# Performance work log

Measured on AMD Instinct MI355X. Metric: run time of the kernel, lower is better.

Reference implementation:

```python
import jax, jax.numpy as jnp
import numpy as np

GRID_SIZE = 64            # scene grid cells at pitch
PITCH = 0.02              # data['resolution']
RES = 0.04                # mast3r_grid_resolution
MAX_PTS = 16              # max_points_in_voxel
MIN_PTS = 15              # min_points_in_voxel
G = int(round(GRID_SIZE * PITCH / RES))   # mast3r grid cells per dim = 32
NUM_VOX = G * G * G                       # 32768
N = 8 * 384 * 512                         # num_images * H * W flattened points


def setup_inputs():
    key = jax.random.key(0)
    k1, k2, k3, k4, k5 = jax.random.split(key, 5)
    half = GRID_SIZE * PITCH / 2 * 1.25   # sample slightly beyond cube -> some out-of-bounds
    pts_0 = jax.random.uniform(k1, (N, 3), jnp.float32, -half, half)
    pts_conf = jax.random.uniform(k2, (N, 1), jnp.float32)
    pts_desc = jax.random.normal(k3, (N, 24), jnp.float32)
    pts_desc_conf = jax.random.uniform(k4, (N, 1), jnp.float32)
    image_ids = jax.random.randint(k5, (N,), 0, 16, jnp.int32)
    center = jnp.zeros((3,), jnp.float32)
    occupancy_grid = jnp.zeros((1, G, G, G), jnp.int32)
    return {"pts_0": pts_0, "pts_conf": pts_conf, "pts_desc": pts_desc,
            "pts_desc_conf": pts_desc_conf, "image_ids": image_ids,
            "center": center, "occupancy_grid": occupancy_grid}


def _voxelize(pts_0, pts_conf, pts_desc, pts_desc_conf, image_ids, center):
    # Hard voxelization with per-voxel point cap, confidence-priority ordering.
    # Fixed-shape (jit-friendly) version: dropped points are masked (zeroed / -1),
    # sentinel bucket NUM_VOX holds out-of-bounds / filtered points.
    n = pts_0.shape[0]
    cube = GRID_SIZE * PITCH
    min_corner = center - cube / 2
    idx = jnp.floor((pts_0 - min_corner) / RES).astype(jnp.int32)
    in_b = jnp.all((idx >= 0) & (idx < G), axis=-1)
    vid = idx[:, 0] * (G * G) + idx[:, 1] * G + idx[:, 2]
    vid = jnp.where(in_b, vid, NUM_VOX)
    ones = jnp.ones((n,), jnp.int32)
    counts0 = jax.ops.segment_sum(ones, vid, num_segments=NUM_VOX + 1)  # bincount
    keep = in_b & (counts0[vid] > MIN_PTS)      # min_points_in_voxel filter
    vid = jnp.where(keep, vid, NUM_VOX)
    # local coords normalized to [-1, 1] within the voxel
    pts_local = (pts_0 - min_corner - idx.astype(pts_0.dtype) * RES - RES / 2) / (RES / 2)
    # stable sort by confidence, descending
    order1 = jnp.argsort(-pts_conf[:, 0], stable=True)
    conf_sorted = pts_conf[order1]
    vid1 = vid[order1]
    # stable sort by voxel id, ascending -> within a voxel, points ordered by conf
    order2 = jnp.argsort(vid1, stable=True)
    vid_sorted = vid1[order2]
    point_sorted = order1[order2]               # indices into original point arrays
    counts = jax.ops.segment_sum(ones, vid_sorted, num_segments=NUM_VOX + 1)
    offsets = jnp.cumsum(counts) - counts
    pos = jnp.arange(n, dtype=jnp.int32) - offsets[vid_sorted].astype(jnp.int32)
    valid = (pos < MAX_PTS) & (vid_sorted < NUM_VOX)   # cap points per voxel
    row = jnp.where(valid, vid_sorted, NUM_VOX)
    col = jnp.clip(pos, 0, MAX_PTS - 1)
    table = jnp.full((NUM_VOX + 1, MAX_PTS), -1, jnp.int32)
    table = table.at[row, col].set(jnp.arange(n, dtype=jnp.int32))[:NUM_VOX]
    vf = valid.astype(pts_0.dtype)
    pts_out = pts_local[point_sorted] * vf[:, None]
    # faithful to source quirk: conf was sorted in place then indexed by point ids
    conf_out = conf_sorted[point_sorted] * vf[:, None]
    desc_out = pts_desc[point_sorted] * vf[:, None]
    desc_conf_out = pts_desc_conf[point_sorted] * vf[:, None]
    img_out = jnp.where(valid, image_ids[point_sorted], -1)
    occupied = (table[:, 0] >= 0).astype(jnp.int32)    # padded analogue of voxel_ids_final
    return pts_out, conf_out, desc_out, desc_conf_out, table, occupied, img_out


def reference(pts_0, pts_conf, pts_desc, pts_desc_conf, image_ids, center, occupancy_grid):
    X = _voxelize(pts_0, pts_conf, pts_desc, pts_desc_conf, image_ids, center)
    return X + (occupancy_grid,)
```

## Files before the change

kernel.cpp:

```cpp
#include <hip/hip_runtime.h>


#define NG 32
#define NVOXEL 32768
#define TILE 4096
#define VCAP 8192
#define CCAP 8192

typedef float v4f __attribute__((ext_vector_type(4)));

__device__ __forceinline__ int conf_bucket(float c) {
  int b = (int)(c * 65536.0f);
  return b < 0 ? 0 : (b > 65535 ? 65535 : b);
}

__device__ int block_scan_excl(int v, int* lds) {
  int t = threadIdx.x;
  lds[t] = v;
  __syncthreads();
  for (int off = 1; off < (int)blockDim.x; off <<= 1) {
    int x = (t >= off) ? lds[t - off] : 0;
    __syncthreads();
    lds[t] += x;
    __syncthreads();
  }
  int incl = lds[t];
  __syncthreads();
  return incl - v;
}

__global__ __launch_bounds__(256) void k_hist(int n, const float* __restrict__ pts,
                                              const float* __restrict__ conf,
                                              const float* __restrict__ center,
                                              unsigned short* __restrict__ code,
                                              int* __restrict__ blockHistV,
                                              int* __restrict__ blockHistC) {
  __shared__ int vh[256], ch[256];
  int t = threadIdx.x;
  vh[t] = 0; ch[t] = 0;
  __syncthreads();
  int base = blockIdx.x * TILE;
  float mx = center[0] - 0.64f, my = center[1] - 0.64f, mz = center[2] - 0.64f;
  for (int r = 0; r < TILE; r += 256) {
    int p = base + r + t;
    if (p < n) {
      float x = pts[3 * p], y = pts[3 * p + 1], z = pts[3 * p + 2];
      int ix = (int)floorf((x - mx) / 0.04f);
      int iy = (int)floorf((y - my) / 0.04f);
      int iz = (int)floorf((z - mz) / 0.04f);
      bool inb = (ix >= 0 && ix < NG && iy >= 0 && iy < NG && iz >= 0 && iz < NG);
      int vid = inb ? (ix * 1024 + iy * 32 + iz) : 0xFFFF;
      code[p] = (unsigned short)vid;
      if (inb) atomicAdd(&vh[vid >> 7], 1);
      atomicAdd(&ch[conf_bucket(conf[p]) >> 8], 1);
    }
  }
  __syncthreads();
  blockHistV[blockIdx.x * 256 + t] = vh[t];
  blockHistC[blockIdx.x * 256 + t] = ch[t];
}

__global__ void k_binprefix(int nblk, const int* __restrict__ blockHistV,
                            const int* __restrict__ blockHistC, int* __restrict__ blockBaseV,
                            int* __restrict__ blockBaseC, int* __restrict__ totals) {
  __shared__ int lds[512];
  int t = threadIdx.x;
  int bin = blockIdx.x & 255;
  int isConf = blockIdx.x >> 8;
  const int* src = isConf ? blockHistC : blockHistV;
  int* dst = isConf ? blockBaseC : blockBaseV;
  int v = (t < nblk) ? src[t * 256 + bin] : 0;
  int ex = block_scan_excl(v, lds);
  if (t < nblk) dst[t * 256 + bin] = ex;
  if (t == nblk - 1) totals[blockIdx.x] = ex + v;
}

__global__ __launch_bounds__(256) void k_scatter(int n, const unsigned short* __restrict__ code,
                                                 const float* __restrict__ conf,
                                                 const int* __restrict__ totals,
                                                 const int* __restrict__ blockBaseV,
                                                 const int* __restrict__ blockBaseC,
                                                 uint2* __restrict__ vidSeg,
                                                 float* __restrict__ confSeg) {
  __shared__ int curV[256], curC[256], lds[256];
  int t = threadIdx.x;
  int exV = block_scan_excl(totals[t], lds);
  int exC = block_scan_excl(totals[256 + t], lds);
  curV[t] = exV + blockBaseV[blockIdx.x * 256 + t];
  curC[t] = exC + blockBaseC[blockIdx.x * 256 + t];
  __syncthreads();
  int base = blockIdx.x * TILE;
  for (int r = 0; r < TILE; r += 256) {
    int p = base + r + t;
    if (p < n) {
      int vid = code[p];
      float c = conf[p];
      int cb = conf_bucket(c);
      if (vid != 0xFFFF) {
        int loc = atomicAdd(&curV[vid >> 7], 1);
        vidSeg[loc] = make_uint2(((unsigned)p << 7) | (unsigned)(vid & 127),
                                 __float_as_uint(c));
      }
      int loc2 = atomicAdd(&curC[cb >> 8], 1);
      confSeg[loc2] = c;
    }
  }
}

__global__ __launch_bounds__(256) void k_voxconf(int n, const uint2* __restrict__ vidSeg,
                                                 const float* __restrict__ confSeg,
                                                 const int* __restrict__ totals,
                                                 uint2* __restrict__ ptlist2,
                                                 int* __restrict__ counts0,
                                                 int* __restrict__ rawOff,
                                                 float* __restrict__ confSorted) {
  __shared__ uint2 seg[VCAP];
  __shared__ int cnt[257], off2[257], scan_t[256];
  __shared__ int s0_sh;
  int t = threadIdx.x;
  if (blockIdx.x < 256) {
    int b = blockIdx.x;
    int ex = block_scan_excl(totals[t], scan_t);
    if (t == b) s0_sh = ex;
    if (t < 128) cnt[t] = 0;
    __syncthreads();
    int s0 = s0_sh;
    int m = totals[b];
    if (m > VCAP) m = VCAP;
    for (int e = t; e < m; e += 256) {
      uint2 pk = vidSeg[s0 + e];
      seg[e] = pk;
      atomicAdd(&cnt[pk.x & 127u], 1);
    }
    __syncthreads();
    int c = (t < 128) ? cnt[t] : 0;
    int ex2 = block_scan_excl(c, scan_t);
    if (t < 128) {
      off2[t] = ex2;
      counts0[b * 128 + t] = c;
      rawOff[b * 128 + t] = s0 + ex2;
      cnt[t] = 0;
    }
    __syncthreads();
    for (int e = t; e < m; e += 256) {
      uint2 pk = seg[e];
      int v = (int)(pk.x & 127u);
      int loc = atomicAdd(&cnt[v], 1);
      ptlist2[s0 + off2[v] + loc] = make_uint2(pk.x >> 7, pk.y);
    }
  } else {
    int b = blockIdx.x - 256;
    float* A = (float*)seg;
    float* B = A + CCAP;
    int ex = block_scan_excl(totals[256 + t], scan_t);
    if (t == b) s0_sh = ex;
    cnt[t] = 0;
    __syncthreads();
    int s0 = s0_sh;
    int m = totals[256 + b];
    if (m > CCAP) m = CCAP;
    for (int e = t; e < m; e += 256) {
      float c = confSeg[s0 + e];
      A[e] = c;
      atomicAdd(&cnt[conf_bucket(c) & 255], 1);
    }
    __syncthreads();
    int ex2 = block_scan_excl(cnt[t], scan_t);
    off2[t] = ex2;
    if (t == 0) off2[256] = m;
    cnt[t] = 0;
    __syncthreads();
    for (int e = t; e < m; e += 256) {
      float c = A[e];
      int f = conf_bucket(c) & 255;
      int loc = atomicAdd(&cnt[f], 1);
      B[off2[f] + loc] = c;
    }
    __syncthreads();
    for (int e = t; e < m; e += 256) {
      int lo = 0, hi = 255;
      while (lo < hi) { int mid = (lo + hi + 1) >> 1; if (off2[mid] <= e) lo = mid; else hi = mid - 1; }
      int fend = off2[lo + 1];
      float v = B[e];
      int rank = 0;
      for (int q = off2[lo]; q < fend; q++) {
        float w = B[q];
        rank += (w > v || (w == v && q < e)) ? 1 : 0;
      }
      A[(m - fend) + rank] = v;
    }
    __syncthreads();
    int dstBase = n - (s0 + m);
    for (int e = t; e < m; e += 256) confSorted[dstBase + e] = A[e];
  }
}

__global__ void k_scan_vox(const int* __restrict__ counts0, int* __restrict__ filtOff,
                           int* __restrict__ filtTotal) {
  __shared__ int lds[1024];
  int t = threadIdx.x;
  int base = t * 32;
  int sf = 0;
  for (int k = 0; k < 32; k++) {
    int c = counts0[base + k];
    sf += (c > 15) ? c : 0;
  }
  int ef = block_scan_excl(sf, lds);
  for (int k = 0; k < 32; k++) {
    int c = counts0[base + k];
    filtOff[base + k] = ef;
    ef += (c > 15) ? c : 0;
  }
  if (t == 1023) filtTotal[0] = ef;
}

__global__ __launch_bounds__(256) void k_select(const int* __restrict__ counts0,
                                                const int* __restrict__ rawOff,
                                                const int* __restrict__ filtOff,
                                                const uint2* __restrict__ ptlist2,
                                                int* __restrict__ rowPoint) {
  __shared__ float lc[4 * 256];
  __shared__ int li[4 * 256];
  int wave = threadIdx.x >> 6, lane = threadIdx.x & 63;
  int v = blockIdx.x * 4 + wave;
  int m = counts0[v];
  bool active = (m > 15);
  int base = rawOff[v];
  int staged = m < 256 ? m : 256;
  float* LC = &lc[wave * 256];
  int* LI = &li[wave * 256];
  if (active) {
    for (int e = lane; e < staged; e += 64) {
      uint2 pk = ptlist2[base + e];
      LI[e] = (int)pk.x;
      LC[e] = __uint_as_float(pk.y);
    }
  }
  __syncthreads();
  if (active) {
    int out0 = filtOff[v];
    for (int e = lane; e < m; e += 64) {
      int pe; float ce;
      if (e < staged) { pe = LI[e]; ce = LC[e]; }
      else { uint2 pk = ptlist2[base + e]; pe = (int)pk.x; ce = __uint_as_float(pk.y); }
      int rank = 0;
      for (int q = 0; q < m; q++) {
        float cq; int pq;
        if (q < staged) { cq = LC[q]; pq = LI[q]; }
        else { uint2 pk = ptlist2[base + q]; pq = (int)pk.x; cq = __uint_as_float(pk.y); }
        rank += (cq > ce || (cq == ce && pq < pe)) ? 1 : 0;
      }
      rowPoint[out0 + rank] = (rank < 16) ? pe : -1;
    }
  }
}

__global__ __launch_bounds__(256) void k_emit(
    int n, const int* __restrict__ rowPoint, const int* __restrict__ filtTotal,
    const float* __restrict__ pts, const float* __restrict__ confSorted,
    const float* __restrict__ dconf, const int* __restrict__ imgid,
    const v4f* __restrict__ desc, const float* __restrict__ center,
    const int* __restrict__ counts0, const int* __restrict__ filtOff,
    const int* __restrict__ occ_in, float* __restrict__ pts_out,
    float* __restrict__ conf_out, v4f* __restrict__ desc_out,
    float* __restrict__ dconf_out, float* __restrict__ table_out,
    float* __restrict__ occupied_out, float* __restrict__ img_out,
    float* __restrict__ occgrid_out) {
  int j = blockIdx.x * blockDim.x + threadIdx.x;
  int T = filtTotal[0];
  if (j < 6 * n) {
    int i = j / 6, c = j - 6 * i;
    int p = (i < T) ? rowPoint[i] : -1;
    v4f val = {0.f, 0.f, 0.f, 0.f};
    if (p >= 0) val = desc[p * 6 + c];
    __builtin_nontemporal_store(val, &desc_out[j]);
    return;
  }
  int j2 = j - 6 * n;
  if (j2 < 3 * n) {
    int i = j2 / 3, c = j2 - 3 * i;
    int p = (i < T) ? rowPoint[i] : -1;
    float o = 0.0f;
    if (p >= 0) {
      float mc = center[c] - 0.64f;
      float x = pts[3 * p + c];
      float fx = floorf((x - mc) / 0.04f);
      o = (x - mc - fx * 0.04f - 0.02f) / 0.02f;
    }
    __builtin_nontemporal_store(o, &pts_out[j2]);
    return;
  }
  j2 -= 3 * n;
  if (j2 < n) {
    int p = (j2 < T) ? rowPoint[j2] : -1;
    float o = (p >= 0) ? confSorted[p] : 0.0f;
    __builtin_nontemporal_store(o, &conf_out[j2]);
    return;
  }
  j2 -= n;
  if (j2 < n) {
    int p = (j2 < T) ? rowPoint[j2] : -1;
    float o = (p >= 0) ? dconf[p] : 0.0f;
    __builtin_nontemporal_store(o, &dconf_out[j2]);
    return;
  }
  j2 -= n;
  if (j2 < n) {
    int p = (j2 < T) ? rowPoint[j2] : -1;
    float o = (p >= 0) ? (float)imgid[p] : -1.0f;
    __builtin_nontemporal_store(o, &img_out[j2]);
    return;
  }
  j2 -= n;
  if (j2 < NVOXEL * 16) {
    int v = j2 >> 4, c = j2 & 15;
    bool occ = counts0[v] > 15;
    float o = occ ? (float)(filtOff[v] + c) : -1.0f;
    __builtin_nontemporal_store(o, &table_out[j2]);
    return;
  }
  j2 -= NVOXEL * 16;
  if (j2 < NVOXEL) {
    float o = (counts0[j2] > 15) ? 1.0f : 0.0f;
    __builtin_nontemporal_store(o, &occupied_out[j2]);
    return;
  }
  j2 -= NVOXEL;
  if (j2 < NVOXEL) {
    float o = (float)occ_in[j2];
    __builtin_nontemporal_store(o, &occgrid_out[j2]);
  }
}

extern "C" void kernel_launch(void* const* d_in, const int* in_sizes, int n_in,
                              void* d_out, int out_size, void* d_ws, size_t ws_size,
                              hipStream_t stream) {
  const int N = in_sizes[0] / 3;
  const float* pts   = (const float*)d_in[0];
  const float* conf  = (const float*)d_in[1];
  const float* desc  = (const float*)d_in[2];
  const float* dconf = (const float*)d_in[3];
  const int* imgid   = (const int*)d_in[4];
  const float* center = (const float*)d_in[5];
  const int* occg    = (const int*)d_in[6];

  float* out = (float*)d_out;
  float* pts_out      = out;
  float* conf_out     = out + (size_t)3 * N;
  float* desc_out     = out + (size_t)4 * N;
  float* dconf_out    = out + (size_t)28 * N;
  float* table_out    = out + (size_t)29 * N;
  float* occupied_out = table_out + (size_t)NVOXEL * 16;
  float* img_out      = occupied_out + NVOXEL;
  float* occgrid_out  = img_out + N;

  const int nTiles = (N + TILE - 1) / TILE;

  char* w = (char*)d_ws;
  uint2* vidSeg    = (uint2*)w;    w += (size_t)N * 8;
  uint2* ptlist2   = (uint2*)w;    w += (size_t)N * 8;
  float* confSeg   = (float*)w;    w += (size_t)N * 4;
  float* confSort  = (float*)w;    w += (size_t)N * 4;
  int* rowPoint    = (int*)w;      w += (size_t)N * 4;
  unsigned short* code = (unsigned short*)w; w += (size_t)N * 2;
  w = (char*)(((size_t)w + 255) & ~(size_t)255);
  int* counts0     = (int*)w;      w += (size_t)NVOXEL * 4;
  int* rawOff      = (int*)w;      w += (size_t)NVOXEL * 4;
  int* filtOff     = (int*)w;      w += (size_t)NVOXEL * 4;
  int* blockHistV  = (int*)w;      w += (size_t)nTiles * 256 * 4;
  int* blockHistC  = (int*)w;      w += (size_t)nTiles * 256 * 4;
  int* blockBaseV  = (int*)w;      w += (size_t)nTiles * 256 * 4;
  int* blockBaseC  = (int*)w;      w += (size_t)nTiles * 256 * 4;
  int* totals      = (int*)w;      w += 512 * 4;
  int* filtTotal   = (int*)w;      w += 4;

  const int B = 256;

  k_hist<<<nTiles, B, 0, stream>>>(N, pts, conf, center, code, blockHistV, blockHistC);
  k_binprefix<<<512, 512, 0, stream>>>(nTiles, blockHistV, blockHistC, blockBaseV, blockBaseC,
                                       totals);
  k_scatter<<<nTiles, B, 0, stream>>>(N, code, conf, totals, blockBaseV, blockBaseC,
                                      vidSeg, confSeg);
  k_voxconf<<<512, B, 0, stream>>>(N, vidSeg, confSeg, totals, ptlist2, counts0, rawOff,
                                   confSort);
  k_scan_vox<<<1, 1024, 0, stream>>>(counts0, filtOff, filtTotal);
  k_select<<<NVOXEL / 4, 256, 0, stream>>>(counts0, rawOff, filtOff, ptlist2, rowPoint);

  const long long totalJ = 12LL * N + (long long)NVOXEL * 16 + 2LL * NVOXEL;
  const int gE = (int)((totalJ + B - 1) / B);
  k_emit<<<gE, B, 0, stream>>>(N, rowPoint, filtTotal, pts, confSort, dconf, imgid,
                               (const v4f*)desc, center, counts0, filtOff, occg, pts_out,
                               conf_out, (v4f*)desc_out, dconf_out, table_out, occupied_out,
                               img_out, occgrid_out);
}
```

Measured before the change: 209.9 us.

## Fuse filtered voxel scan into voxconf/select and add nontemporal loads

Removes the single-block k_scan_vox launch. Each voxconf bin block now computes a local exclusive scan of filtered counts plus a per-bin total. Every k_select block rescans the 256 bin totals to recover global filtered offsets, and also writes filtOff and filtTotal. Streaming reads of segment buffers and gathered inputs are switched to nontemporal loads. This cuts a serial one-block kernel and a launch, at the cost of a redundant 256-element scan in every select block.

Result: slower. 217.4 us (+3.5%).

```diff
diff --git a/kernel.cpp b/kernel.cpp
--- a/kernel.cpp
+++ b/kernel.cpp
@@ -8,6 +8,7 @@
 #define CCAP 8192
 
 typedef float v4f __attribute__((ext_vector_type(4)));
+typedef unsigned v2u __attribute__((ext_vector_type(2)));
 
 __device__ __forceinline__ int conf_bucket(float c) {
   int b = (int)(c * 65536.0f);
@@ -113,6 +114,8 @@
                                                  uint2* __restrict__ ptlist2,
                                                  int* __restrict__ counts0,
                                                  int* __restrict__ rawOff,
+                                                 int* __restrict__ filtLocal,
+                                                 int* __restrict__ filtBinTot,
                                                  float* __restrict__ confSorted) {
   __shared__ uint2 seg[VCAP];
   __shared__ int cnt[257], off2[257], scan_t[256];
@@ -128,19 +131,24 @@
     int m = totals[b];
     if (m > VCAP) m = VCAP;
     for (int e = t; e < m; e += 256) {
-      uint2 pk = vidSeg[s0 + e];
+      v2u pk2 = __builtin_nontemporal_load((const v2u*)&vidSeg[s0 + e]);
+      uint2 pk = make_uint2(pk2.x, pk2.y);
       seg[e] = pk;
       atomicAdd(&cnt[pk.x & 127u], 1);
     }
     __syncthreads();
     int c = (t < 128) ? cnt[t] : 0;
     int ex2 = block_scan_excl(c, scan_t);
+    int cf = (c > 15) ? c : 0;
+    int exf = block_scan_excl(cf, scan_t);
     if (t < 128) {
       off2[t] = ex2;
       counts0[b * 128 + t] = c;
       rawOff[b * 128 + t] = s0 + ex2;
+      filtLocal[b * 128 + t] = exf;
       cnt[t] = 0;
     }
+    if (t == 127) filtBinTot[b] = exf + cf;
     __syncthreads();
     for (int e = t; e < m; e += 256) {
       uint2 pk = seg[e];
@@ -160,7 +168,7 @@
     int m = totals[256 + b];
     if (m > CCAP) m = CCAP;
     for (int e = t; e < m; e += 256) {
-      float c = confSeg[s0 + e];
+      float c = __builtin_nontemporal_load(&confSeg[s0 + e]);
       A[e] = c;
       atomicAdd(&cnt[conf_bucket(c) & 255], 1);
     }
@@ -195,37 +203,30 @@
   }
 }
 
-__global__ void k_scan_vox(const int* __restrict__ counts0, int* __restrict__ filtOff,
-                           int* __restrict__ filtTotal) {
-  __shared__ int lds[1024];
-  int t = threadIdx.x;
-  int base = t * 32;
-  int sf = 0;
-  for (int k = 0; k < 32; k++) {
-    int c = counts0[base + k];
-    sf += (c > 15) ? c : 0;
-  }
-  int ef = block_scan_excl(sf, lds);
-  for (int k = 0; k < 32; k++) {
-    int c = counts0[base + k];
-    filtOff[base + k] = ef;
-    ef += (c > 15) ? c : 0;
-  }
-  if (t == 1023) filtTotal[0] = ef;
-}
-
 __global__ __launch_bounds__(256) void k_select(const int* __restrict__ counts0,
                                                 const int* __restrict__ rawOff,
-                                                const int* __restrict__ filtOff,
+                                                const int* __restrict__ filtLocal,
+                                                const int* __restrict__ filtBinTot,
                                                 const uint2* __restrict__ ptlist2,
+                                                int* __restrict__ filtOff,
+                                                int* __restrict__ filtTotal,
                                                 int* __restrict__ rowPoint) {
   __shared__ float lc[4 * 256];
   __shared__ int li[4 * 256];
+  __shared__ int scan_t[256], bb[256];
+  int t = threadIdx.x;
+  int fb = filtBinTot[t];
+  int exb = block_scan_excl(fb, scan_t);
+  bb[t] = exb;
+  if (blockIdx.x == 0 && t == 255) filtTotal[0] = exb + fb;
+  __syncthreads();
   int wave = threadIdx.x >> 6, lane = threadIdx.x & 63;
   int v = blockIdx.x * 4 + wave;
   int m = counts0[v];
   bool active = (m > 15);
   int base = rawOff[v];
+  int out0 = bb[v >> 7] + filtLocal[v];
+  if (lane == 0) filtOff[v] = out0;
   int staged = m < 256 ? m : 256;
   float* LC = &lc[wave * 256];
   int* LI = &li[wave * 256];
@@ -238,7 +239,6 @@
   }
   __syncthreads();
   if (active) {
-    int out0 = filtOff[v];
     for (int e = lane; e < m; e += 64) {
       int pe; float ce;
       if (e < staged) { pe = LI[e]; ce = LC[e]; }
@@ -272,7 +272,7 @@
     int i = j / 6, c = j - 6 * i;
     int p = (i < T) ? rowPoint[i] : -1;
     v4f val = {0.f, 0.f, 0.f, 0.f};
-    if (p >= 0) val = desc[p * 6 + c];
+    if (p >= 0) val = __builtin_nontemporal_load(&desc[p * 6 + c]);
     __builtin_nontemporal_store(val, &desc_out[j]);
     return;
   }
@@ -300,14 +300,14 @@
   j2 -= n;
   if (j2 < n) {
     int p = (j2 < T) ? rowPoint[j2] : -1;
-    float o = (p >= 0) ? dconf[p] : 0.0f;
+    float o = (p >= 0) ? __builtin_nontemporal_load(&dconf[p]) : 0.0f;
     __builtin_nontemporal_store(o, &dconf_out[j2]);
     return;
   }
   j2 -= n;
   if (j2 < n) {
     int p = (j2 < T) ? rowPoint[j2] : -1;
-    float o = (p >= 0) ? (float)imgid[p] : -1.0f;
+    float o = (p >= 0) ? (float)__builtin_nontemporal_load(&imgid[p]) : -1.0f;
     __builtin_nontemporal_store(o, &img_out[j2]);
     return;
   }
@@ -367,11 +367,13 @@
   int* counts0     = (int*)w;      w += (size_t)NVOXEL * 4;
   int* rawOff      = (int*)w;      w += (size_t)NVOXEL * 4;
   int* filtOff     = (int*)w;      w += (size_t)NVOXEL * 4;
+  int* filtLocal   = (int*)w;      w += (size_t)NVOXEL * 4;
   int* blockHistV  = (int*)w;      w += (size_t)nTiles * 256 * 4;
   int* blockHistC  = (int*)w;      w += (size_t)nTiles * 256 * 4;
   int* blockBaseV  = (int*)w;      w += (size_t)nTiles * 256 * 4;
   int* blockBaseC  = (int*)w;      w += (size_t)nTiles * 256 * 4;
   int* totals      = (int*)w;      w += 512 * 4;
+  int* filtBinTot  = (int*)w;      w += 256 * 4;
   int* filtTotal   = (int*)w;      w += 4;
 
   const int B = 256;
@@ -382,9 +384,9 @@
   k_scatter<<<nTiles, B, 0, stream>>>(N, code, conf, totals, blockBaseV, blockBaseC,
                                       vidSeg, confSeg);
   k_voxconf<<<512, B, 0, stream>>>(N, vidSeg, confSeg, totals, ptlist2, counts0, rawOff,
-                                   confSort);
-  k_scan_vox<<<1, 1024, 0, stream>>>(counts0, filtOff, filtTotal);
-  k_select<<<NVOXEL / 4, 256, 0, stream>>>(counts0, rawOff, filtOff, ptlist2, rowPoint);
+                                   filtLocal, filtBinTot, confSort);
+  k_select<<<NVOXEL / 4, 256, 0, stream>>>(counts0, rawOff, filtLocal, filtBinTot, ptlist2,
+                                           filtOff, filtTotal, rowPoint);
 
   const long long totalJ = 12LL * N + (long long)NVOXEL * 16 + 2LL * NVOXEL;
   const int gE = (int)((totalJ + B - 1) / B);
```
